# Performance work log

Hardware: AMD Instinct MI355X
Metric: run time of the kernel (lower is better)

## Reference

```python
import jax, jax.numpy as jnp
import numpy as np

B, T, D, HD = 4, 4096, 1024, 64

def setup_inputs() -> dict:
    key = jax.random.key(0)
    k1, k2, k3, k4 = jax.random.split(key, 4)
    scale = 1.0 / np.sqrt(D)
    return {
        "x": jax.random.normal(k1, (B, T, D), dtype=jnp.float32),
        "Wq": jax.random.normal(k2, (HD, D), dtype=jnp.float32) * scale,
        "Wk": jax.random.normal(k3, (HD, D), dtype=jnp.float32) * scale,
        "Wv": jax.random.normal(k4, (HD, D), dtype=jnp.float32) * scale,
    }

def reference(x, Wq, Wk, Wv):
    # x: [B,T,D]; W*: [head_dim, D] (torch Linear weight layout)
    Q = jnp.einsum('btd,hd->bth', x, Wq)  # [B,T,HD]
    K = jnp.einsum('btd,hd->bth', x, Wk)
    V = jnp.einsum('btd,hd->bth', x, Wv)
    hd = Q.shape[-1]
    scores = jnp.einsum('bqh,bkh->bqk', Q, K) * (hd ** -0.5)  # [B,T,T]
    t = scores.shape[1]
    causal = jnp.tril(jnp.ones((t, t), dtype=bool))
    scores = jnp.where(causal, scores, -jnp.inf)
    att = jax.nn.softmax(scores, axis=-1)
    return jnp.einsum('bqk,bkh->bqh', att, V)  # [B,T,HD]
```

## Files before the change

kernel.cpp:

```cpp
#include <hip/hip_runtime.h>
#include <stdint.h>

#define B_  4
#define T_  4096
#define D_  1024
#define HD_ 64
#define BT_ 16384

typedef short bf16x8 __attribute__((ext_vector_type(8)));
typedef float f32x4  __attribute__((ext_vector_type(4)));
typedef unsigned short u16;
typedef u16 u16x4 __attribute__((ext_vector_type(4)));

#define M0_ 8.0f

__device__ __forceinline__ u16 f2bf(float f) {
    union { float f; unsigned u; } v; v.f = f;
    unsigned r = (v.u + 0x7FFF + ((v.u >> 16) & 1)) >> 16;
    return (u16)r;
}
__device__ __forceinline__ float bf2f(u16 u) {
    union { unsigned u; float f; } v; v.u = ((unsigned)u) << 16;
    return v.f;
}

__device__ __forceinline__ int slot_base(int qt) {
    int a = qt >> 4, r = qt & 15;
    return qt + 8 * a * (a - 1) + a * r;
}

__global__ __launch_bounds__(256) void wconv_kernel(
    const float* __restrict__ wq, const float* __restrict__ wk,
    const float* __restrict__ wv, u16* __restrict__ wb)
{
    const int j   = blockIdx.x >> 5;
    const int off = (blockIdx.x & 31) * 2048 + threadIdx.x * 8;
    const float* src = (j == 0) ? wq : ((j == 1) ? wk : wv);
    f32x4 a0 = *(const f32x4*)(src + off);
    f32x4 a1 = *(const f32x4*)(src + off + 4);
    bf16x8 b;
    #pragma unroll
    for (int i = 0; i < 4; ++i) { b[i] = (short)f2bf(a0[i]); b[4 + i] = (short)f2bf(a1[i]); }
    *(bf16x8*)(wb + j * 65536 + off) = b;
}

__global__ __launch_bounds__(256) void qkv_kernel(
    const float* __restrict__ x, const u16* __restrict__ wb,
    u16* __restrict__ qs, u16* __restrict__ kss, u16* __restrict__ vssT)
{
    __shared__ __align__(16) u16 xt[32][72];
    __shared__ __align__(16) u16 wt[192][72];

    const int tid  = threadIdx.x;
    const int lane = tid & 63;
    const int w    = tid >> 6;
    const int quad = lane >> 4;
    const int l16  = lane & 15;
    const int row0 = blockIdx.x * 32;
    const int sp   = w >> 1;
    const int gh   = (w & 1) * 6;

    const int xrow = tid >> 3;
    const int xcg  = tid & 7;

    f32x4 acc[6];
    #pragma unroll
    for (int g = 0; g < 6; ++g) acc[g] = (f32x4)0.0f;

    f32x4 xa, xb;
    bf16x8 wr[6];
    {
        const float* xp = x + (size_t)(row0 + xrow) * D_ + xcg * 8;
        xa = *(const f32x4*)xp; xb = *(const f32x4*)(xp + 4);
        #pragma unroll
        for (int i = 0; i < 6; ++i) {
            int chunk = tid + 256 * i;
            wr[i] = *(const bf16x8*)(wb + (size_t)(chunk >> 3) * D_ + (chunk & 7) * 8);
        }
    }

    for (int kc = 0; kc < 16; ++kc) {
        __syncthreads();
        {
            bf16x8 px;
            #pragma unroll
            for (int i = 0; i < 4; ++i) { px[i] = (short)f2bf(xa[i]); px[4 + i] = (short)f2bf(xb[i]); }
            *(bf16x8*)&xt[xrow][xcg * 8] = px;
            #pragma unroll
            for (int i = 0; i < 6; ++i) {
                int chunk = tid + 256 * i;
                *(bf16x8*)&wt[chunk >> 3][(chunk & 7) * 8] = wr[i];
            }
        }
        __syncthreads();
        if (kc < 15) {
            const float* xp = x + (size_t)(row0 + xrow) * D_ + (kc + 1) * 64 + xcg * 8;
            xa = *(const f32x4*)xp; xb = *(const f32x4*)(xp + 4);
            #pragma unroll
            for (int i = 0; i < 6; ++i) {
                int chunk = tid + 256 * i;
                wr[i] = *(const bf16x8*)(wb + (size_t)(chunk >> 3) * D_ + (kc + 1) * 64 + (chunk & 7) * 8);
            }
        }
        #pragma unroll
        for (int ks = 0; ks < 2; ++ks) {
            bf16x8 a = *(const bf16x8*)&xt[sp * 16 + l16][ks * 32 + quad * 8];
            #pragma unroll
            for (int g = 0; g < 6; ++g) {
                bf16x8 b = *(const bf16x8*)&wt[(gh + g) * 16 + l16][ks * 32 + quad * 8];
                acc[g] = __builtin_amdgcn_mfma_f32_16x16x32_bf16(a, b, acc[g], 0, 0, 0);
            }
        }
    }
    #pragma unroll
    for (int g = 0; g < 6; ++g) {
        const int n = (gh + g) * 16 + l16;
        const int j = n >> 6, h = n & 63;
        const int rbase = row0 + sp * 16 + quad * 4;
        if (j == 0) {
            #pragma unroll
            for (int r = 0; r < 4; ++r) qs[(size_t)(rbase + r) * HD_ + h] = f2bf(acc[g][r] * 0.125f);
        } else if (j == 1) {
            #pragma unroll
            for (int r = 0; r < 4; ++r) kss[(size_t)(rbase + r) * HD_ + h] = f2bf(acc[g][r]);
        } else {
            u16x4 v;
            #pragma unroll
            for (int r = 0; r < 4; ++r) v[r] = f2bf(acc[g][r]);
            *(u16x4*)(vssT + (size_t)h * BT_ + rbase) = v;
        }
    }
}

__global__ __launch_bounds__(256) void attn_kernel(
    const u16* __restrict__ qs, const u16* __restrict__ kss,
    const u16* __restrict__ vssT,
    float* __restrict__ pl, u16* __restrict__ pO)
{
    __shared__ __align__(16) u16 kt[64][72];
    __shared__ __align__(16) u16 vt[80][72];
    __shared__ __align__(16) u16 pt[4][16][72];

    const int bi = blockIdx.x;
    const int c  = bi & 3;
    const int qt = (bi >> 2) & 63;
    const int b  = bi >> 8;
    if ((c << 4) > qt) return;

    const int kt0  = c << 4;
    const int kend = ((kt0 + 15) < qt) ? (kt0 + 15) : qt;

    const int tid  = threadIdx.x;
    const int lane = tid & 63;
    const int w    = tid >> 6;
    const int quad = lane >> 4;
    const int l16  = lane & 15;
    const int qb   = qt * 64;
    const size_t base = (size_t)b * T_;

    for (int idx = tid; idx < 16 * 72; idx += 256) {
        int rr = idx / 72, cc = idx - rr * 72;
        vt[64 + rr][cc] = (rr == 0) ? (u16)0x3F80 : (u16)0;
    }

    bf16x8 qf[2];
    {
        const u16* qp = qs + (base + qb + w * 16 + l16) * HD_ + quad * 8;
        qf[0] = *(const bf16x8*)(qp);
        qf[1] = *(const bf16x8*)(qp + 32);
    }

    f32x4 o_acc[5];
    #pragma unroll
    for (int g = 0; g < 5; ++g) o_acc[g] = (f32x4)0.0f;

    const int lr = tid >> 2, lp = tid & 3;

    bf16x8 kr0, kr1, vr0, vr1;
    {
        const u16* sk = kss + (base + kt0 * 64 + lr) * HD_ + lp * 16;
        kr0 = *(const bf16x8*)(sk);  kr1 = *(const bf16x8*)(sk + 8);
        const u16* sv = vssT + (size_t)lr * BT_ + base + kt0 * 64 + lp * 16;
        vr0 = *(const bf16x8*)(sv);  vr1 = *(const bf16x8*)(sv + 8);
    }

    for (int kti = kt0; kti <= kend; ++kti) {
        __syncthreads();
        *(bf16x8*)&kt[lr][lp * 16]     = kr0;
        *(bf16x8*)&kt[lr][lp * 16 + 8] = kr1;
        *(bf16x8*)&vt[lr][lp * 16]     = vr0;
        *(bf16x8*)&vt[lr][lp * 16 + 8] = vr1;
        __syncthreads();
        if (kti < kend) {
            const u16* sk = kss + (base + (kti + 1) * 64 + lr) * HD_ + lp * 16;
            kr0 = *(const bf16x8*)(sk);  kr1 = *(const bf16x8*)(sk + 8);
            const u16* sv = vssT + (size_t)lr * BT_ + base + (kti + 1) * 64 + lp * 16;
            vr0 = *(const bf16x8*)(sv);  vr1 = *(const bf16x8*)(sv + 8);
        }

        f32x4 s[4];
        #pragma unroll
        for (int g = 0; g < 4; ++g) {
            s[g] = (f32x4)0.0f;
            #pragma unroll
            for (int ks = 0; ks < 2; ++ks) {
                bf16x8 kf = *(const bf16x8*)&kt[g * 16 + l16][ks * 32 + quad * 8];
                s[g] = __builtin_amdgcn_mfma_f32_16x16x32_bf16(qf[ks], kf, s[g], 0, 0, 0);
            }
        }
        if (kti == qt) {
            #pragma unroll
            for (int g = 0; g < 4; ++g) {
                int key = kti * 64 + g * 16 + l16;
                #pragma unroll
                for (int r = 0; r < 4; ++r) {
                    int q = qb + w * 16 + quad * 4 + r;
                    if (key > q) s[g][r] = -1e30f;
                }
            }
        }
        #pragma unroll
        for (int g = 0; g < 4; ++g)
            #pragma unroll
            for (int r = 0; r < 4; ++r)
                pt[w][quad * 4 + r][g * 16 + l16] = f2bf(__expf(s[g][r] - M0_));
        #pragma unroll
        for (int ks = 0; ks < 2; ++ks) {
            bf16x8 pa = *(const bf16x8*)&pt[w][l16][ks * 32 + quad * 8];
            #pragma unroll
            for (int g = 0; g < 5; ++g) {
                bf16x8 vf = *(const bf16x8*)&vt[g * 16 + l16][ks * 32 + quad * 8];
                o_acc[g] = __builtin_amdgcn_mfma_f32_16x16x32_bf16(pa, vf, o_acc[g], 0, 0, 0);
            }
        }
    }

    const int slot = b * 160 + slot_base(qt) + c;
    if (l16 == 0) {
        #pragma unroll
        for (int r = 0; r < 4; ++r)
            pl[slot * 64 + w * 16 + quad * 4 + r] = o_acc[4][r];
    }
    #pragma unroll
    for (int g = 0; g < 4; ++g) {
        #pragma unroll
        for (int r = 0; r < 4; ++r) {
            int row = w * 16 + quad * 4 + r;
            pO[(size_t)slot * 4096 + row * 64 + g * 16 + l16] = f2bf(o_acc[g][r]);
        }
    }
}

__global__ __launch_bounds__(256) void merge_kernel(
    const float* __restrict__ pl, const u16* __restrict__ pO,
    float* __restrict__ out)
{
    const int bi = blockIdx.x;
    const int qt = bi & 63, b = bi >> 6;
    const int nc = (qt >> 4) + 1;
    const int s0 = b * 160 + slot_base(qt);
    const int row = threadIdx.x >> 2;
    const int hg  = (threadIdx.x & 3) * 16;

    float L = 0.0f;
    for (int c2 = 0; c2 < nc; ++c2) L += pl[(s0 + c2) * 64 + row];

    float o[16];
    #pragma unroll
    for (int i = 0; i < 16; ++i) o[i] = 0.0f;
    for (int c2 = 0; c2 < nc; ++c2) {
        const u16* p = pO + (size_t)(s0 + c2) * 4096 + row * 64 + hg;
        bf16x8 v0 = *(const bf16x8*)p;
        bf16x8 v1 = *(const bf16x8*)(p + 8);
        #pragma unroll
        for (int i = 0; i < 8; ++i) {
            o[i]     += bf2f((u16)v0[i]);
            o[8 + i] += bf2f((u16)v1[i]);
        }
    }
    const float inv = 1.0f / L;
    float* op = out + ((size_t)b * T_ + qt * 64 + row) * HD_ + hg;
    #pragma unroll
    for (int j = 0; j < 4; ++j) {
        f32x4 v;
        #pragma unroll
        for (int i = 0; i < 4; ++i) v[i] = o[j * 4 + i] * inv;
        *(f32x4*)(op + j * 4) = v;
    }
}

extern "C" void kernel_launch(void* const* d_in, const int* in_sizes, int n_in,
                              void* d_out, int out_size, void* d_ws, size_t ws_size,
                              hipStream_t stream) {
    const float* x  = (const float*)d_in[0];
    const float* wq = (const float*)d_in[1];
    const float* wk = (const float*)d_in[2];
    const float* wv = (const float*)d_in[3];

    const size_t NE = (size_t)BT_ * HD_;
    char* ws = (char*)d_ws;
    u16* qs   = (u16*)ws;
    u16* kss  = qs  + NE;
    u16* vssT = kss + NE;
    u16* wb   = vssT + NE;
    float* pl = (float*)(wb + 192 * 1024);
    u16* pO   = (u16*)(pl + 640 * 64);
    float* out = (float*)d_out;

    wconv_kernel<<<dim3(96),   dim3(256), 0, stream>>>(wq, wk, wv, wb);
    qkv_kernel  <<<dim3(512),  dim3(256), 0, stream>>>(x, wb, qs, kss, vssT);
    attn_kernel <<<dim3(1024), dim3(256), 0, stream>>>(qs, kss, vssT, pl, pO);
    merge_kernel<<<dim3(256),  dim3(256), 0, stream>>>(pl, pO, out);
}
```

Before: 154.3 us.

## Split attention key range into smaller chunks and use packed bf16 conversion

```diff
diff --git a/kernel.cpp b/kernel.cpp
--- a/kernel.cpp
+++ b/kernel.cpp
@@ -11,8 +11,14 @@
 typedef float f32x4  __attribute__((ext_vector_type(4)));
 typedef unsigned short u16;
 typedef u16 u16x4 __attribute__((ext_vector_type(4)));
-
-#define M0_ 8.0f
+typedef unsigned int u32;
+typedef u32 u32x4 __attribute__((ext_vector_type(4)));
+
+#define M0_   8.0f
+#define L2E_  1.44269504f
+#define M0L2_ 11.54156032f
+
+#define SLOTS_B_ 288
 
 __device__ __forceinline__ u16 f2bf(float f) {
     union { float f; unsigned u; } v; v.f = f;
@@ -23,10 +29,15 @@
     union { unsigned u; float f; } v; v.u = ((unsigned)u) << 16;
     return v.f;
 }
+__device__ __forceinline__ u32 cvt_pk_bf16(float lo, float hi) {
+    u32 r;
+    asm("v_cvt_pk_bf16_f32 %0, %1, %2" : "=v"(r) : "v"(lo), "v"(hi));
+    return r;
+}
 
 __device__ __forceinline__ int slot_base(int qt) {
-    int a = qt >> 4, r = qt & 15;
-    return qt + 8 * a * (a - 1) + a * r;
+    int a = qt >> 3, r = qt & 7;
+    return qt + 4 * a * (a - 1) + a * r;
 }
 
 __global__ __launch_bounds__(256) void wconv_kernel(
@@ -38,10 +49,12 @@
     const float* src = (j == 0) ? wq : ((j == 1) ? wk : wv);
     f32x4 a0 = *(const f32x4*)(src + off);
     f32x4 a1 = *(const f32x4*)(src + off + 4);
-    bf16x8 b;
-    #pragma unroll
-    for (int i = 0; i < 4; ++i) { b[i] = (short)f2bf(a0[i]); b[4 + i] = (short)f2bf(a1[i]); }
-    *(bf16x8*)(wb + j * 65536 + off) = b;
+    u32x4 b;
+    b[0] = cvt_pk_bf16(a0[0], a0[1]);
+    b[1] = cvt_pk_bf16(a0[2], a0[3]);
+    b[2] = cvt_pk_bf16(a1[0], a1[1]);
+    b[3] = cvt_pk_bf16(a1[2], a1[3]);
+    *(u32x4*)(wb + j * 65536 + off) = b;
 }
 
 __global__ __launch_bounds__(256) void qkv_kernel(
@@ -82,10 +95,12 @@
     for (int kc = 0; kc < 16; ++kc) {
         __syncthreads();
         {
-            bf16x8 px;
-            #pragma unroll
-            for (int i = 0; i < 4; ++i) { px[i] = (short)f2bf(xa[i]); px[4 + i] = (short)f2bf(xb[i]); }
-            *(bf16x8*)&xt[xrow][xcg * 8] = px;
+            u32x4 px;
+            px[0] = cvt_pk_bf16(xa[0], xa[1]);
+            px[1] = cvt_pk_bf16(xa[2], xa[3]);
+            px[2] = cvt_pk_bf16(xb[0], xb[1]);
+            px[3] = cvt_pk_bf16(xb[2], xb[3]);
+            *(u32x4*)&xt[xrow][xcg * 8] = px;
             #pragma unroll
             for (int i = 0; i < 6; ++i) {
                 int chunk = tid + 256 * i;
@@ -142,13 +157,13 @@
     __shared__ __align__(16) u16 pt[4][16][72];
 
     const int bi = blockIdx.x;
-    const int c  = bi & 3;
-    const int qt = (bi >> 2) & 63;
-    const int b  = bi >> 8;
-    if ((c << 4) > qt) return;
-
-    const int kt0  = c << 4;
-    const int kend = ((kt0 + 15) < qt) ? (kt0 + 15) : qt;
+    const int c  = bi & 7;
+    const int qt = (bi >> 3) & 63;
+    const int b  = bi >> 9;
+    if ((c << 3) > qt) return;
+
+    const int kt0  = c << 3;
+    const int kend = ((kt0 + 7) < qt) ? (kt0 + 7) : qt;
 
     const int tid  = threadIdx.x;
     const int lane = tid & 63;
@@ -220,10 +235,16 @@
             }
         }
         #pragma unroll
-        for (int g = 0; g < 4; ++g)
-            #pragma unroll
-            for (int r = 0; r < 4; ++r)
-                pt[w][quad * 4 + r][g * 16 + l16] = f2bf(__expf(s[g][r] - M0_));
+        for (int g = 0; g < 4; ++g) {
+            #pragma unroll
+            for (int r = 0; r < 4; r += 2) {
+                float e0 = __builtin_amdgcn_exp2f(s[g][r]     * L2E_ - M0L2_);
+                float e1 = __builtin_amdgcn_exp2f(s[g][r + 1] * L2E_ - M0L2_);
+                u32 pk = cvt_pk_bf16(e0, e1);
+                pt[w][quad * 4 + r][g * 16 + l16]     = (u16)pk;
+                pt[w][quad * 4 + r + 1][g * 16 + l16] = (u16)(pk >> 16);
+            }
+        }
         #pragma unroll
         for (int ks = 0; ks < 2; ++ks) {
             bf16x8 pa = *(const bf16x8*)&pt[w][l16][ks * 32 + quad * 8];
@@ -235,7 +256,7 @@
         }
     }
 
-    const int slot = b * 160 + slot_base(qt) + c;
+    const int slot = b * SLOTS_B_ + slot_base(qt) + c;
     if (l16 == 0) {
         #pragma unroll
         for (int r = 0; r < 4; ++r)
@@ -256,37 +277,35 @@
     float* __restrict__ out)
 {
     const int bi = blockIdx.x;
-    const int qt = bi & 63, b = bi >> 6;
-    const int nc = (qt >> 4) + 1;
-    const int s0 = b * 160 + slot_base(qt);
-    const int row = threadIdx.x >> 2;
-    const int hg  = (threadIdx.x & 3) * 16;
+    const int rh = bi & 1;
+    const int qt = (bi >> 1) & 63;
+    const int b  = bi >> 7;
+    const int nc = (qt >> 3) + 1;
+    const int s0 = b * SLOTS_B_ + slot_base(qt);
+    const int row = rh * 32 + (threadIdx.x >> 3);
+    const int hg  = (threadIdx.x & 7) * 8;
 
     float L = 0.0f;
     for (int c2 = 0; c2 < nc; ++c2) L += pl[(s0 + c2) * 64 + row];
 
-    float o[16];
-    #pragma unroll
-    for (int i = 0; i < 16; ++i) o[i] = 0.0f;
+    float o[8];
+    #pragma unroll
+    for (int i = 0; i < 8; ++i) o[i] = 0.0f;
     for (int c2 = 0; c2 < nc; ++c2) {
         const u16* p = pO + (size_t)(s0 + c2) * 4096 + row * 64 + hg;
         bf16x8 v0 = *(const bf16x8*)p;
-        bf16x8 v1 = *(const bf16x8*)(p + 8);
-        #pragma unroll
-        for (int i = 0; i < 8; ++i) {
-            o[i]     += bf2f((u16)v0[i]);
-            o[8 + i] += bf2f((u16)v1[i]);
-        }
+        #pragma unroll
+        for (int i = 0; i < 8; ++i) o[i] += bf2f((u16)v0[i]);
     }
     const float inv = 1.0f / L;
     float* op = out + ((size_t)b * T_ + qt * 64 + row) * HD_ + hg;
-    #pragma unroll
-    for (int j = 0; j < 4; ++j) {
-        f32x4 v;
-        #pragma unroll
-        for (int i = 0; i < 4; ++i) v[i] = o[j * 4 + i] * inv;
-        *(f32x4*)(op + j * 4) = v;
-    }
+    f32x4 v;
+    #pragma unroll
+    for (int i = 0; i < 4; ++i) v[i] = o[i] * inv;
+    *(f32x4*)op = v;
+    #pragma unroll
+    for (int i = 0; i < 4; ++i) v[i] = o[4 + i] * inv;
+    *(f32x4*)(op + 4) = v;
 }
 
 extern "C" void kernel_launch(void* const* d_in, const int* in_sizes, int n_in,
@@ -304,11 +323,11 @@
     u16* vssT = kss + NE;
     u16* wb   = vssT + NE;
     float* pl = (float*)(wb + 192 * 1024);
-    u16* pO   = (u16*)(pl + 640 * 64);
+    u16* pO   = (u16*)(pl + 4 * SLOTS_B_ * 64);
     float* out = (float*)d_out;
 
     wconv_kernel<<<dim3(96),   dim3(256), 0, stream>>>(wq, wk, wv, wb);
     qkv_kernel  <<<dim3(512),  dim3(256), 0, stream>>>(x, wb, qs, kss, vssT);
-    attn_kernel <<<dim3(1024), dim3(256), 0, stream>>>(qs, kss, vssT, pl, pO);
-    merge_kernel<<<dim3(256),  dim3(256), 0, stream>>>(pl, pO, out);
-}
+    attn_kernel <<<dim3(2048), dim3(256), 0, stream>>>(qs, kss, vssT, pl, pO);
+    merge_kernel<<<dim3(512),  dim3(256), 0, stream>>>(pl, pO, out);
+}
```

New measurement: 154.1 us. No clear change (-0.1%).
